# Optimization experiments

Hardware: AMD Instinct MI355X
Metric: run time of the kernel (lower is better)

Reference implementation:

```python
import jax, jax.numpy as jnp
import numpy as np

EPS = 1e-5
MAXN = 1.0 - 1e-5
SEG, T_HORIZONS, MARGIN = 24, 4, 0.1

# --- Poincare ball (c=1) ops ---

def _norm(x):
    return jnp.sqrt(jnp.clip(jnp.sum(x * x, -1, keepdims=True), EPS * EPS, None))

def projx(x):
    n = jnp.sqrt(jnp.clip(jnp.sum(x * x, -1, keepdims=True), EPS * EPS, None))
    return jnp.where(n > MAXN, x * (MAXN / n), x)

def mobius_add(x, y):
    x2 = jnp.sum(x * x, -1, keepdims=True)
    y2 = jnp.sum(y * y, -1, keepdims=True)
    xy = jnp.sum(x * y, -1, keepdims=True)
    num = (1 + 2 * xy + y2) * x + (1 - x2) * y
    den = 1 + 2 * xy + x2 * y2
    return num / jnp.maximum(den, EPS)

def lam(x):
    return 2.0 / jnp.clip(1 - jnp.sum(x * x, -1, keepdims=True), EPS, None)

def expmap(x, v):
    vn = _norm(v)
    return projx(mobius_add(x, jnp.tanh(0.5 * lam(x) * vn) * v / vn))

def logmap(x, y):
    u = mobius_add(-x, y)
    un = _norm(u)
    return (2.0 / lam(x)) * jnp.arctanh(jnp.clip(un, None, MAXN)) * u / un

def expmap0(v):
    vn = _norm(v)
    return projx(jnp.tanh(vn) * v / vn)

def logmap0(x):
    xn = _norm(x)
    return jnp.arctanh(jnp.clip(xn, None, MAXN)) * x / xn

def mob_smul(r, x):
    xn = _norm(x)
    return projx(jnp.tanh(r * jnp.arctanh(jnp.clip(xn, None, MAXN))) * x / xn)

def dist0(x):
    n = jnp.sqrt(jnp.clip(jnp.sum(x * x, -1), EPS * EPS, None))
    return 2.0 * jnp.arctanh(jnp.clip(n, None, MAXN))


def setup_inputs() -> dict:
    key = jax.random.key(0)
    ks = jax.random.split(key, 8)
    B, L, F, D, H = 32, 336, 256, 128, 256
    r = lambda k, s, sc: jax.random.normal(k, s, jnp.float32) * sc
    return {
        "trend": r(ks[0], (B, L, F), 1.0),
        "seasonal_coarse": r(ks[1], (B, L, F), 1.0),
        "seasonal_fine": r(ks[2], (B, L, F), 1.0),
        "residual": r(ks[3], (B, L, F), 1.0),
        "revin_w": jnp.ones((F,), jnp.float32),
        "revin_b": jnp.zeros((F,), jnp.float32),
        "enc_W": r(ks[4], (4, SEG, D), 0.05),
        "enc_b": jnp.zeros((4, D), jnp.float32),
        "vel_W": r(ks[5], (4, D, D), 0.05),
        "vel_b": jnp.zeros((4, D), jnp.float32),
        "steps": jnp.ones((4,), jnp.float32),
        "mobius_w": jnp.full((4,), 0.25, jnp.float32),
        "rec_W1": r(ks[6], (D, H), 0.05),
        "rec_b1": jnp.zeros((H,), jnp.float32),
        "rec_W2": r(ks[7], (H, SEG), 0.05),
        "rec_b2": jnp.zeros((SEG,), jnp.float32),
    }


def reference(trend, seasonal_coarse, seasonal_fine, residual, revin_w, revin_b,
              enc_W, enc_b, vel_W, vel_b, steps, mobius_w,
              rec_W1, rec_b1, rec_W2, rec_b2):
    B, L, F = trend.shape
    N = L // SEG
    # RevIN stats on the combined signal
    x = trend + seasonal_coarse + seasonal_fine + residual
    mean = jnp.mean(x, 1, keepdims=True)                    # [B,1,F]
    std = jnp.sqrt(jnp.var(x, 1, keepdims=True) + 1e-5)

    def collapse(c):
        cn = ((c - 0.25 * mean) / std) * revin_w + 0.25 * revin_b
        return jnp.transpose(cn, (0, 2, 1)).reshape(B * F, N, SEG)

    comps = jnp.stack([collapse(trend), collapse(seasonal_coarse),
                       collapse(seasonal_fine), collapse(residual)])  # [4,BF,N,SEG]

    def branch(xs, We, be, Wv, bv, s):
        z = projx(expmap0(xs @ We + be))                    # [BF,N,D] latents on ball
        v = logmap(z[:, :-1], z[:, 1:])                     # [BF,N-1,D]
        w = 0.9 ** (N - 2 - jnp.arange(N - 1, dtype=xs.dtype))
        w = w / w.sum()
        v_init = jnp.mean(v * w[None, :, None], axis=1)     # weighted then .mean, as in torch
        v0t = projx(expmap0(logmap0(v_init) @ Wv + bv))     # PoincareLinear
        ts = jnp.arange(1, T_HORIZONS + 1, dtype=xs.dtype)
        v_t = jax.nn.sigmoid(s) * ts[None, :, None] * v0t[:, None, :]  # [BF,T,D]
        return expmap(z[:, -1][:, None, :], v_t)            # [BF,T,D]

    z_fut = jax.vmap(branch)(comps, enc_W, enc_b, vel_W, vel_b, steps)  # [4,BF,T,D]

    # Mobius fusion
    w = jax.nn.softmax(mobius_w)
    comb = mob_smul(w[0], z_fut[0])
    for i in range(1, 4):
        comb = mobius_add(comb, mob_smul(w[i], z_fut[i]))
    comb = projx(comb)

    # Reconstruction head: logmap0 -> MLP -> segment values
    h = jax.nn.relu(logmap0(comb) @ rec_W1 + rec_b1)
    seg_out = h @ rec_W2 + rec_b2                           # [BF,T,SEG]
    pred_n = seg_out.reshape(B, F, T_HORIZONS * SEG).transpose(0, 2, 1)  # [B,pred_len,F]
    pred = (pred_n - revin_b) / revin_w * std + mean        # RevIN denorm

    # Hierarchical margin loss on distances from origin
    d = dist0(z_fut)                                        # [4,BF,T]
    hloss = (jnp.mean(jax.nn.relu(d[0] - d[1] + MARGIN)) +
             jnp.mean(jax.nn.relu(d[1] - d[2] + MARGIN)) +
             jnp.mean(jax.nn.relu(d[2] - d[3] + MARGIN)))
    return pred, hloss
```

## Files before the change

### kernel.cpp

```cpp
#include <hip/hip_runtime.h>
#include <math.h>

#define EPSF 1e-5f
#define MAXNF (1.0f - 1e-5f)

constexpr int SEGc = 24;
constexpr int Nn   = 14;
constexpr int NS   = Nn * SEGc;
constexpr int Tt   = 4;
constexpr int Bb   = 32;
constexpr int Ll   = 336;
constexpr int Ff   = 256;
constexpr int Dd   = 128;
constexpr int Hh   = 256;
constexpr int BFc  = Bb * Ff;

constexpr float WNORM = 1.0f / (7.458134171670999f * 13.0f);
constexpr float LN09  = -0.10536051565782628f;

typedef float v2f __attribute__((ext_vector_type(2)));
__device__ __forceinline__ v2f vset(float a, float b){ v2f r; r.x=a; r.y=b; return r; }
__device__ __forceinline__ v2f vsplat(float s){ v2f r; r.x=s; r.y=s; return r; }
__device__ __forceinline__ v2f vfma(v2f a, v2f b, v2f c){
#if __has_builtin(__builtin_elementwise_fma)
    return __builtin_elementwise_fma(a, b, c);
#else
    return vset(fmaf(a.x, b.x, c.x), fmaf(a.y, b.y, c.y));
#endif
}
__device__ __forceinline__ v2f vfmas(float a, v2f b, v2f c){ return vfma(vsplat(a), b, c); }

__device__ __forceinline__ float frcp(float x)  { return __builtin_amdgcn_rcpf(x); }
__device__ __forceinline__ float fsqrtf_(float x){ return __builtin_amdgcn_sqrtf(x); }
__device__ __forceinline__ float ftanh_pos(float x) {
    const float e = __expf(fminf(2.f * x, 30.f));
    return (e - 1.f) * frcp(e + 1.f);
}
__device__ __forceinline__ float fatanh01(float x) {
    return 0.5f * __logf((1.f + x) * frcp(1.f - x));
}

__global__ __launch_bounds__(256, 4) void fused_kernel(
    const float* __restrict__ trend, const float* __restrict__ scoarse,
    const float* __restrict__ sfine, const float* __restrict__ resid,
    const float* __restrict__ revin_w, const float* __restrict__ revin_b,
    const float* __restrict__ enc_W, const float* __restrict__ enc_b,
    const float* __restrict__ vel_W, const float* __restrict__ vel_b,
    const float* __restrict__ steps, const float* __restrict__ mobius_w,
    const float* __restrict__ rec_W1, const float* __restrict__ rec_b1,
    const float* __restrict__ rec_W2, const float* __restrict__ rec_b2,
    float* __restrict__ out, float* __restrict__ hpart)
{
    const int bid   = blockIdx.x;
    const int kpair = ((bid & 7) << 9) | (bid >> 3);
    const int bf0   = kpair << 1;
    const int b     = bf0 >> 8;
    const int f0    = bf0 & 255;
    const int tid   = threadIdx.x;
    const int wid   = tid >> 6;
    const int lane  = tid & 63;
    const int gi    = lane & 15;
    const int pg    = (lane >> 4) & 1;

    __shared__ float lds_big[2 * 4 * Tt * Dd];
    __shared__ float bcu[8 * Dd];
    __shared__ float zfns[2][4][Tt];
    __shared__ float red[16];

#define XS(p, c)     (lds_big + ((p) * 4 + (c)) * NS)
#define ZFL(p, i, t) (lds_big + (((p) * 4 + (i)) * Tt + (t)) * Dd)

    const float* cp = (wid == 0) ? trend : (wid == 1) ? scoarse
                    : (wid == 2) ? sfine : resid;

#pragma unroll 1
    for (int i = lane; i < NS; i += 64) {
        const float2 v = *reinterpret_cast<const float2*>(&cp[(b * Ll + i) * Ff + f0]);
        XS(0, wid)[i] = v.x;
        XS(1, wid)[i] = v.y;
    }
    __syncthreads();

    float s0 = 0.f, q0 = 0.f, s1 = 0.f, q1 = 0.f;
#pragma unroll 1
    for (int l = tid; l < NS; l += 256) {
        const float x0 = XS(0,0)[l] + XS(0,1)[l] + XS(0,2)[l] + XS(0,3)[l];
        const float x1 = XS(1,0)[l] + XS(1,1)[l] + XS(1,2)[l] + XS(1,3)[l];
        s0 += x0; q0 += x0 * x0; s1 += x1; q1 += x1 * x1;
    }
#pragma unroll 1
    for (int off = 1; off < 64; off <<= 1) {
        s0 += __shfl_xor(s0, off, 64); q0 += __shfl_xor(q0, off, 64);
        s1 += __shfl_xor(s1, off, 64); q1 += __shfl_xor(q1, off, 64);
    }
    if (lane == 0) {
        red[wid] = s0; red[4 + wid] = q0; red[8 + wid] = s1; red[12 + wid] = q1;
    }
    __syncthreads();
    s0 = red[0] + red[1] + red[2] + red[3];
    q0 = red[4] + red[5] + red[6] + red[7];
    s1 = red[8] + red[9] + red[10] + red[11];
    q1 = red[12] + red[13] + red[14] + red[15];
    const float mean0 = s0 * (1.f / (float)NS);
    const float stdv0 = fsqrtf_(q0 * (1.f / (float)NS) - mean0 * mean0 + 1e-5f);
    const float mean1 = s1 * (1.f / (float)NS);
    const float stdv1 = fsqrtf_(q1 * (1.f / (float)NS) - mean1 * mean1 + 1e-5f);
    const float rw0v = revin_w[f0],     rb0v = revin_b[f0];
    const float rw1v = revin_w[f0 + 1], rb1v = revin_b[f0 + 1];
    const float aff0 = frcp(stdv0) * rw0v;
    const float kaf0 = 0.25f * (rb0v - mean0 * aff0);
    const float aff1 = frcp(stdv1) * rw1v;
    const float kaf1 = 0.25f * (rb1v - mean1 * aff1);

    const int c = wid;
    const float4* xv40 = reinterpret_cast<const float4*>(XS(0, c));
    const float4* xv41 = reinterpret_cast<const float4*>(XS(1, c));
    const float* Wep = enc_W + c * SEGc * Dd + 2 * lane;
    const float* Wvp = vel_W + c * Dd * Dd + 2 * lane;

    v2f wreg[SEGc];
#pragma unroll
    for (int s = 0; s < SEGc; ++s)
        wreg[s] = *reinterpret_cast<const v2f*>(Wep + s * Dd);
    const v2f bev = *reinterpret_cast<const v2f*>(enc_b + c * Dd + 2 * lane);
    const v2f bvv = *reinterpret_cast<const v2f*>(vel_b + c * Dd + 2 * lane);

    v2f csv = vsplat(0.f);
#pragma unroll
    for (int s = 0; s < SEGc; ++s) csv += wreg[s];
    const v2f kb0v = vfmas(kaf0, csv, bev);
    const v2f kb1v = vfmas(kaf1, csv, bev);

    v2f y0v[Nn], y1v[Nn];
#pragma unroll
    for (int n = 0; n < Nn; ++n) {
        v2f a0 = vsplat(0.f), a1 = vsplat(0.f);
#pragma unroll
        for (int q = 0; q < SEGc / 4; ++q) {
            const float4 xa = xv40[n * (SEGc / 4) + q];
            const float4 xb = xv41[n * (SEGc / 4) + q];
            a0 = vfmas(xa.x, wreg[4*q+0], a0); a1 = vfmas(xb.x, wreg[4*q+0], a1);
            a0 = vfmas(xa.y, wreg[4*q+1], a0); a1 = vfmas(xb.y, wreg[4*q+1], a1);
            a0 = vfmas(xa.z, wreg[4*q+2], a0); a1 = vfmas(xb.z, wreg[4*q+2], a1);
            a0 = vfmas(xa.w, wreg[4*q+3], a0); a1 = vfmas(xb.w, wreg[4*q+3], a1);
        }
        y0v[n] = vfmas(aff0, a0, kb0v);
        y1v[n] = vfmas(aff1, a1, kb1v);
    }

    float qnv[2][Nn], rdv[2][Nn - 1];
#pragma unroll
    for (int n = 0; n < Nn; ++n) {
        qnv[0][n] = fmaf(y0v[n].y, y0v[n].y, y0v[n].x * y0v[n].x);
        qnv[1][n] = fmaf(y1v[n].y, y1v[n].y, y1v[n].x * y1v[n].x);
    }
#pragma unroll
    for (int n = 1; n < Nn; ++n) {
        rdv[0][n - 1] = fmaf(y0v[n-1].y, y0v[n].y, y0v[n-1].x * y0v[n].x);
        rdv[1][n - 1] = fmaf(y1v[n-1].y, y1v[n].y, y1v[n-1].x * y1v[n].x);
    }
#pragma unroll 1
    for (int off = 1; off < 64; off <<= 1) {
#pragma unroll
        for (int n = 0; n < Nn; ++n) {
            qnv[0][n] += __shfl_xor(qnv[0][n], off, 64);
            qnv[1][n] += __shfl_xor(qnv[1][n], off, 64);
        }
#pragma unroll
        for (int j = 0; j < Nn - 1; ++j) {
            rdv[0][j] += __shfl_xor(rdv[0][j], off, 64);
            rdv[1][j] += __shfl_xor(rdv[1][j], off, 64);
        }
    }
    float qsel0 = qnv[0][0], qsel1 = qnv[1][0];
#pragma unroll
    for (int n = 1; n < Nn; ++n) {
        qsel0 = (gi == n) ? qnv[0][n] : qsel0;
        qsel1 = (gi == n) ? qnv[1][n] : qsel1;
    }
    const float qn_own = pg ? qsel1 : qsel0;
    float rsel0 = rdv[0][0], rsel1 = rdv[1][0];
#pragma unroll
    for (int n = 1; n < Nn - 1; ++n) {
        rsel0 = (gi == n) ? rdv[0][n] : rsel0;
        rsel1 = (gi == n) ? rdv[1][n] : rsel1;
    }
    const float rd_own = pg ? rsel1 : rsel0;

    const float vn = fsqrtf_(fmaxf(qn_own, EPSF * EPSF));
    const float th = ftanh_pos(vn);
    float s_own = th * frcp(vn);
    float nrm = th;
    if (nrm > MAXNF) { s_own *= MAXNF * frcp(nrm); nrm = MAXNF; }
    const float zn2_own = nrm * nrm;

    const float s_prev   = __shfl(s_own,   lane - 1, 64);
    const float zn2_prev = __shfl(zn2_own, lane - 1, 64);
    const float rd_prev  = __shfl(rd_own,  lane - 1, 64);

    const float xyv  = -(s_prev * s_own * rd_prev);
    const float x2v  = zn2_prev, yy2 = zn2_own;
    const float c1v  = 1.f + 2.f * xyv + yy2;
    const float c2v  = 1.f - x2v;
    const float rdenv = frcp(fmaxf(1.f + 2.f * xyv + x2v * yy2, EPSF));
    const float un2 = rdenv * rdenv *
        (c1v * c1v * x2v + 2.f * c1v * c2v * xyv + c2v * c2v * yy2);
    const float un  = fsqrtf_(fmaxf(un2, EPSF * EPSF));
    const float lf  = fmaxf(1.f - x2v, EPSF);
    const float gml = lf * fatanh01(fminf(un, MAXNF)) * frcp(un);
    const float wj  = WNORM * __expf(LN09 * (float)(13 - gi));
    const float gw  = wj * gml * rdenv;
    const float g1_own = -gw * c1v * s_prev;
    const float g2_own =  gw * c2v * s_own;

    v2f vi0v = vsplat(0.f), vi1v = vsplat(0.f);
#pragma unroll
    for (int n = 0; n < Nn; ++n) {
        float cf0 = 0.f, cf1 = 0.f;
        if (n >= 1)      { cf0 = __shfl(g2_own, n, 64);       cf1 = __shfl(g2_own, 16 + n, 64); }
        if (n <= Nn - 2) { cf0 += __shfl(g1_own, n + 1, 64);  cf1 += __shfl(g1_own, 17 + n, 64); }
        vi0v = vfmas(cf0, y0v[n], vi0v);
        vi1v = vfmas(cf1, y1v[n], vi1v);
    }
    const float scl0 = __shfl(s_own, 13, 64),  x2l0 = __shfl(zn2_own, 13, 64);
    const float scl1 = __shfl(s_own, 29, 64),  x2l1 = __shfl(zn2_own, 29, 64);
    const v2f z0lv = y0v[Nn-1] * scl0;
    const v2f z1lv = y1v[Nn-1] * scl1;

    float vin20 = fmaf(vi0v.y, vi0v.y, vi0v.x * vi0v.x);
    float vin21 = fmaf(vi1v.y, vi1v.y, vi1v.x * vi1v.x);
#pragma unroll 1
    for (int off = 1; off < 64; off <<= 1) {
        vin20 += __shfl_xor(vin20, off, 64);
        vin21 += __shfl_xor(vin21, off, 64);
    }
    const float vinn0 = fsqrtf_(fmaxf(vin20, EPSF * EPSF));
    const float lgv0  = fatanh01(fminf(vinn0, MAXNF)) * frcp(vinn0);
    const float vinn1 = fsqrtf_(fmaxf(vin21, EPSF * EPSF));
    const float lgv1  = fatanh01(fminf(vinn1, MAXNF)) * frcp(vinn1);
    *reinterpret_cast<v2f*>(&bcu[(0 * 4 + c) * Dd + 2 * lane]) = vi0v * lgv0;
    *reinterpret_cast<v2f*>(&bcu[(4 + c) * Dd + 2 * lane])     = vi1v * lgv1;
    __syncthreads();

    v2f m0v = bvv, m1v = bvv;
    {
        const float4* bc40 = reinterpret_cast<const float4*>(bcu + (0 * 4 + c) * Dd);
        const float4* bc41 = reinterpret_cast<const float4*>(bcu + (4 + c) * Dd);
#pragma unroll 1
        for (int kb = 0; kb < Dd / 8; ++kb) {
            v2f w[8];
#pragma unroll
            for (int r = 0; r < 8; ++r)
                w[r] = *reinterpret_cast<const v2f*>(Wvp + (8 * kb + r) * Dd);
            const float4 ta0 = bc40[2*kb], tb0 = bc40[2*kb+1];
            const float4 ta1 = bc41[2*kb], tb1 = bc41[2*kb+1];
            m0v = vfmas(ta0.x, w[0], m0v); m1v = vfmas(ta1.x, w[0], m1v);
            m0v = vfmas(ta0.y, w[1], m0v); m1v = vfmas(ta1.y, w[1], m1v);
            m0v = vfmas(ta0.z, w[2], m0v); m1v = vfmas(ta1.z, w[2], m1v);
            m0v = vfmas(ta0.w, w[3], m0v); m1v = vfmas(ta1.w, w[3], m1v);
            m0v = vfmas(tb0.x, w[4], m0v); m1v = vfmas(tb1.x, w[4], m1v);
            m0v = vfmas(tb0.y, w[5], m0v); m1v = vfmas(tb1.y, w[5], m1v);
            m0v = vfmas(tb0.z, w[6], m0v); m1v = vfmas(tb1.z, w[6], m1v);
            m0v = vfmas(tb0.w, w[7], m0v); m1v = vfmas(tb1.w, w[7], m1v);
        }
    }
    float mn20 = fmaf(m0v.y, m0v.y, m0v.x * m0v.x);
    float zdm0 = fmaf(z0lv.y, m0v.y, z0lv.x * m0v.x);
    float mn21 = fmaf(m1v.y, m1v.y, m1v.x * m1v.x);
    float zdm1 = fmaf(z1lv.y, m1v.y, z1lv.x * m1v.x);
#pragma unroll 1
    for (int off = 1; off < 64; off <<= 1) {
        mn20 += __shfl_xor(mn20, off, 64); zdm0 += __shfl_xor(zdm0, off, 64);
        mn21 += __shfl_xor(mn21, off, 64); zdm1 += __shfl_xor(zdm1, off, 64);
    }

    const float sig = frcp(1.f + __expf(-steps[c]));
    {
        const float mn2g = pg ? mn21 : mn20;
        const float zdmg = pg ? zdm1 : zdm0;
        const float x2lg = pg ? x2l1 : x2l0;
        const float mng  = fsqrtf_(fmaxf(mn2g, EPSF * EPSF));
        const float thg  = ftanh_pos(mng);
        float sc2g = thg * frcp(mng);
        float v0ng = thg;
        if (v0ng > MAXNF) { sc2g *= MAXNF * frcp(v0ng); v0ng = MAXNF; }
        const float v0n2g  = mn2g * sc2g * sc2g;
        const float zdotvg = sc2g * zdmg;
        const float lamxg  = 2.f * frcp(fmaxf(1.f - x2lg, EPSF));

        const float alpha = sig * (float)(gi + 1);
        const float vtn2  = alpha * alpha * v0n2g;
        const float vtn   = fsqrtf_(fmaxf(vtn2, EPSF * EPSF));
        const float gg    = ftanh_pos(0.5f * lamxg * vtn);
        const float cyc   = gg * alpha * frcp(vtn);
        const float y2    = cyc * cyc * v0n2g;
        const float xy    = cyc * zdotvg;
        const float c1 = 1.f + 2.f * xy + y2;
        const float c2 = 1.f - x2lg;
        const float rden = frcp(fmaxf(1.f + 2.f * xy + x2lg * y2, EPSF));
        float rn2 = rden * rden *
            (c1 * c1 * x2lg + 2.f * c1 * c2 * xy + c2 * c2 * y2);
        float rn = fsqrtf_(fmaxf(rn2, EPSF * EPSF));
        float sclip = 1.f;
        if (rn > MAXNF) { sclip = MAXNF * frcp(rn); rn = MAXNF; }
        const float At_own = c1 * rden * sclip;
        const float Bt_own = c2 * cyc * rden * sclip;
        if (lane < 32 && gi < Tt) zfns[pg][c][gi] = rn;

        const float sc2_0 = __shfl(sc2g, 0, 64), sc2_1 = __shfl(sc2g, 16, 64);
        const v2f v0d0 = m0v * sc2_0;
        const v2f v0d1 = m1v * sc2_1;
#pragma unroll 1
        for (int t = 0; t < Tt; ++t) {
            const float A0 = __shfl(At_own, t, 64),      B0 = __shfl(Bt_own, t, 64);
            const float A1 = __shfl(At_own, 16 + t, 64), B1 = __shfl(Bt_own, 16 + t, 64);
            *reinterpret_cast<v2f*>(ZFL(0, c, t) + 2 * lane) = vfmas(A0, z0lv, v0d0 * B0);
            *reinterpret_cast<v2f*>(ZFL(1, c, t) + 2 * lane) = vfmas(A1, z1lv, v0d1 * B1);
        }
    }
    __syncthreads();

    {
        float mwa = mobius_w[0], mwb = mobius_w[1], mwc = mobius_w[2], mwd = mobius_w[3];
        const float mx = fmaxf(fmaxf(mwa, mwb), fmaxf(mwc, mwd));
        mwa = __expf(mwa - mx); mwb = __expf(mwb - mx);
        mwc = __expf(mwc - mx); mwd = __expf(mwd - mx);
        const float rse = frcp(mwa + mwb + mwc + mwd);
        const float mw[4] = {mwa * rse, mwb * rse, mwc * rse, mwd * rse};

        const int t = wid;
        v2f e0[4], e1[4];
#pragma unroll
        for (int i = 0; i < 4; ++i) {
            e0[i] = *reinterpret_cast<const v2f*>(ZFL(0, i, t) + 2 * lane);
            e1[i] = *reinterpret_cast<const v2f*>(ZFL(1, i, t) + 2 * lane);
        }
        float gp[12];
        gp[0]  = fmaf(e0[0].y, e0[1].y, e0[0].x * e0[1].x);
        gp[1]  = fmaf(e0[0].y, e0[2].y, e0[0].x * e0[2].x);
        gp[2]  = fmaf(e0[0].y, e0[3].y, e0[0].x * e0[3].x);
        gp[3]  = fmaf(e0[1].y, e0[2].y, e0[1].x * e0[2].x);
        gp[4]  = fmaf(e0[1].y, e0[3].y, e0[1].x * e0[3].x);
        gp[5]  = fmaf(e0[2].y, e0[3].y, e0[2].x * e0[3].x);
        gp[6]  = fmaf(e1[0].y, e1[1].y, e1[0].x * e1[1].x);
        gp[7]  = fmaf(e1[0].y, e1[2].y, e1[0].x * e1[2].x);
        gp[8]  = fmaf(e1[0].y, e1[3].y, e1[0].x * e1[3].x);
        gp[9]  = fmaf(e1[1].y, e1[2].y, e1[1].x * e1[2].x);
        gp[10] = fmaf(e1[1].y, e1[3].y, e1[1].x * e1[3].x);
        gp[11] = fmaf(e1[2].y, e1[3].y, e1[2].x * e1[3].x);
#pragma unroll 1
        for (int off = 1; off < 64; off <<= 1) {
#pragma unroll
            for (int k = 0; k < 12; ++k) gp[k] += __shfl_xor(gp[k], off, 64);
        }

        const int il = lane & 3;
        float mwv_own = mw[0];
        mwv_own = (il == 1) ? mw[1] : mwv_own;
        mwv_own = (il == 2) ? mw[2] : mwv_own;
        mwv_own = (il == 3) ? mw[3] : mwv_own;
        const float xn_own = zfns[pg][il][t];
        const float smc = ftanh_pos(mwv_own * fatanh01(xn_own)) * frcp(xn_own);
        float smv[2][4];
#pragma unroll
        for (int i = 0; i < 4; ++i) {
            smv[0][i] = __shfl(smc, i, 64);
            smv[1][i] = __shfl(smc, 16 + i, 64);
        }

#pragma unroll
        for (int p = 0; p < 2; ++p) {
            const float xn0 = zfns[p][0][t], xn1 = zfns[p][1][t];
            const float xn2 = zfns[p][2][t], xn3 = zfns[p][3][t];
            const float Gd[4] = {xn0*xn0, xn1*xn1, xn2*xn2, xn3*xn3};
            const float G[4][4] = {
                {Gd[0], gp[6*p+0], gp[6*p+1], gp[6*p+2]},
                {gp[6*p+0], Gd[1], gp[6*p+3], gp[6*p+4]},
                {gp[6*p+1], gp[6*p+3], Gd[2], gp[6*p+5]},
                {gp[6*p+2], gp[6*p+4], gp[6*p+5], Gd[3]}};
            float a0 = smv[p][0], a1 = 0.f, a2 = 0.f, a3 = 0.f;
            float cn2 = smv[p][0] * smv[p][0] * Gd[0];
#pragma unroll
            for (int i = 1; i < 4; ++i) {
                const float si = smv[p][i];
                const float xy = si * (a0*G[0][i] + a1*G[1][i] + a2*G[2][i] + a3*G[3][i]);
                const float y2 = si * si * Gd[i];
                const float c1 = 1.f + 2.f * xy + y2;
                const float c2 = 1.f - cn2;
                const float rden = frcp(fmaxf(1.f + 2.f * xy + cn2 * y2, EPSF));
                const float f1 = rden * c1, f2 = rden * c2 * si;
                a0 *= f1; a1 *= f1; a2 *= f1; a3 *= f1;
                if (i == 1) a1 += f2; else if (i == 2) a2 += f2; else a3 += f2;
                cn2 = rden * rden * (c1*c1*cn2 + 2.f*c1*c2*xy + c2*c2*y2);
            }
            float cn = fsqrtf_(fmaxf(cn2, EPSF * EPSF));
            float csc = 1.f;
            if (cn > MAXNF) { csc = MAXNF * frcp(cn); cn = MAXNF; }
            const float lg = fatanh01(cn) * frcp(cn) * csc;
            const v2f* ee = p ? e1 : e0;
            v2f uv = ee[0] * a0;
            uv = vfmas(a1, ee[1], uv);
            uv = vfmas(a2, ee[2], uv);
            uv = vfmas(a3, ee[3], uv);
            uv = uv * lg;
            const int ub = (t * Dd + 2 * lane) * 2 + p;
            bcu[ub]     = uv.x;
            bcu[ub + 2] = uv.y;
        }
    }

    if (wid == 0) {
        float ddv = 0.f;
        if (lane < 32)
            ddv = 2.f * fatanh01(zfns[pg][lane & 3][gi >> 2]);
        const float ddn = __shfl(ddv, lane + 1, 64);
        float hv = ((lane < 32) && ((lane & 3) != 3))
                 ? fmaxf(ddv - ddn + 0.1f, 0.f) : 0.f;
#pragma unroll 1
        for (int off = 1; off < 16; off <<= 1) hv += __shfl_xor(hv, off, 64);
        if (lane == 0)  hpart[bf0]     = hv;
        if (lane == 16) hpart[bf0 + 1] = hv;
    }
    __syncthreads();

    {
        const float4* u4 = reinterpret_cast<const float4*>(bcu);
        const float bb = rec_b1[tid];
        v2f accv[4] = {vsplat(bb), vsplat(bb), vsplat(bb), vsplat(bb)};
        const float* w1p = rec_W1 + tid;
#pragma unroll 1
        for (int kb = 0; kb < Dd / 8; ++kb) {
            float wv[8];
#pragma unroll
            for (int r = 0; r < 8; ++r) wv[r] = w1p[(8 * kb + r) * Hh];
#pragma unroll
            for (int rr = 0; rr < 4; ++rr) {
#pragma unroll
                for (int t = 0; t < 4; ++t) {
                    const float4 U = u4[t * (Dd / 2) + 4 * kb + rr];
                    accv[t] = vfmas(wv[2*rr],   vset(U.x, U.y), accv[t]);
                    accv[t] = vfmas(wv[2*rr+1], vset(U.z, U.w), accv[t]);
                }
            }
        }
#pragma unroll
        for (int t = 0; t < 4; ++t) {
            v2f h = vset(fmaxf(accv[t].x, 0.f), fmaxf(accv[t].y, 0.f));
            *reinterpret_cast<v2f*>(lds_big + (t * Hh + tid) * 2) = h;
        }
    }
    __syncthreads();

    if (tid < Tt * SEGc) {
        const int t = tid / SEGc, s = tid - t * SEGc;
        const float4* h4 = reinterpret_cast<const float4*>(lds_big);
        const float* w2p = rec_W2 + s;
        v2f acc2 = vsplat(rec_b2[s]);
#pragma unroll 1
        for (int jb = 0; jb < Hh / 8; ++jb) {
            float wv[8];
#pragma unroll
            for (int r = 0; r < 8; ++r) wv[r] = w2p[(8 * jb + r) * SEGc];
#pragma unroll
            for (int rr = 0; rr < 4; ++rr) {
                const float4 H = h4[t * (Hh / 2) + 4 * jb + rr];
                acc2 = vfmas(wv[2*rr],   vset(H.x, H.y), acc2);
                acc2 = vfmas(wv[2*rr+1], vset(H.z, H.w), acc2);
            }
        }
        const v2f rbv = vset(rb0v, rb1v);
        const v2f rwr = vset(frcp(rw0v), frcp(rw1v));
        const v2f sdv = vset(stdv0, stdv1);
        const v2f mnv = vset(mean0, mean1);
        const v2f res = (acc2 - rbv) * rwr * sdv + mnv;
        *reinterpret_cast<float2*>(&out[(b * (Tt * SEGc) + tid) * Ff + f0]) =
            make_float2(res.x, res.y);
    }
#undef XS
#undef ZFL
}

__global__ __launch_bounds__(256) void hloss_kernel(
    const float* __restrict__ hpart, float* __restrict__ out)
{
    __shared__ float sm[256];
    const int tid = threadIdx.x;
    float s = 0.f;
#pragma unroll 1
    for (int i = tid; i < BFc; i += 256) s += hpart[i];
    sm[tid] = s;
    __syncthreads();
#pragma unroll 1
    for (int off = 128; off > 0; off >>= 1) {
        if (tid < off) sm[tid] += sm[tid + off];
        __syncthreads();
    }
    if (tid == 0) out[Bb * Tt * SEGc * Ff] = sm[0] / (float)(BFc * Tt);
}

extern "C" void kernel_launch(void* const* d_in, const int* in_sizes, int n_in,
                              void* d_out, int out_size, void* d_ws, size_t ws_size,
                              hipStream_t stream) {
    const float* trend   = (const float*)d_in[0];
    const float* scoarse = (const float*)d_in[1];
    const float* sfine   = (const float*)d_in[2];
    const float* resid   = (const float*)d_in[3];
    const float* revin_w = (const float*)d_in[4];
    const float* revin_b = (const float*)d_in[5];
    const float* enc_W   = (const float*)d_in[6];
    const float* enc_b   = (const float*)d_in[7];
    const float* vel_W   = (const float*)d_in[8];
    const float* vel_b   = (const float*)d_in[9];
    const float* steps   = (const float*)d_in[10];
    const float* mobw    = (const float*)d_in[11];
    const float* rec_W1  = (const float*)d_in[12];
    const float* rec_b1  = (const float*)d_in[13];
    const float* rec_W2  = (const float*)d_in[14];
    const float* rec_b2  = (const float*)d_in[15];

    float* out = (float*)d_out;
    float* wsf = (float*)d_ws;

    fused_kernel<<<BFc / 2, 256, 0, stream>>>(
        trend, scoarse, sfine, resid, revin_w, revin_b,
        enc_W, enc_b, vel_W, vel_b, steps, mobw,
        rec_W1, rec_b1, rec_W2, rec_b2,
        out, wsf);
    hloss_kernel<<<1, 256, 0, stream>>>(wsf, out);
}
```

Measured before the change: 221.4 us.

## Have each wave load all four components redundantly to drop block barriers

Every wave now reads all four component inputs for its two features, computes the RevIN sum and sum-of-squares itself with a wave-level reduction, and stores only its own component in a private LDS region. This removes the cross-wave LDS reduction and two __syncthreads, and the LDS layout is changed so that each wave's scratch and z_fut region is separate. In exchange, global load traffic per block is four times higher, though the repeated loads should mostly hit in cache. The barrier before the velocity matvec is also removed, which is safe only because each wave reads only the bcu rows it wrote itself.

```diff
diff --git a/kernel.cpp b/kernel.cpp
--- a/kernel.cpp
+++ b/kernel.cpp
@@ -62,45 +62,42 @@
     const int gi    = lane & 15;
     const int pg    = (lane >> 4) & 1;
 
-    __shared__ float lds_big[2 * 4 * Tt * Dd];
+    __shared__ float lds_big[4 * 1024];
     __shared__ float bcu[8 * Dd];
     __shared__ float zfns[2][4][Tt];
-    __shared__ float red[16];
-
-#define XS(p, c)     (lds_big + ((p) * 4 + (c)) * NS)
-#define ZFL(p, i, t) (lds_big + (((p) * 4 + (i)) * Tt + (t)) * Dd)
-
-    const float* cp = (wid == 0) ? trend : (wid == 1) ? scoarse
-                    : (wid == 2) ? sfine : resid;
-
-#pragma unroll 1
-    for (int i = lane; i < NS; i += 64) {
-        const float2 v = *reinterpret_cast<const float2*>(&cp[(b * Ll + i) * Ff + f0]);
-        XS(0, wid)[i] = v.x;
-        XS(1, wid)[i] = v.y;
-    }
-    __syncthreads();
+
+#define XSW(p)        (lds_big + c * 1024 + (p) * NS)
+#define ZFL2(cc, p, t)(lds_big + (cc) * 1024 + ((p) * 4 + (t)) * Dd)
+
+    const int c = wid;
 
     float s0 = 0.f, q0 = 0.f, s1 = 0.f, q1 = 0.f;
-#pragma unroll 1
-    for (int l = tid; l < NS; l += 256) {
-        const float x0 = XS(0,0)[l] + XS(0,1)[l] + XS(0,2)[l] + XS(0,3)[l];
-        const float x1 = XS(1,0)[l] + XS(1,1)[l] + XS(1,2)[l] + XS(1,3)[l];
-        s0 += x0; q0 += x0 * x0; s1 += x1; q1 += x1 * x1;
+    {
+        float* xs0 = XSW(0);
+        float* xs1 = XSW(1);
+#pragma unroll 1
+        for (int l = lane; l < NS; l += 64) {
+            const int gidx = (b * Ll + l) * Ff + f0;
+            const float2 vt = *reinterpret_cast<const float2*>(&trend[gidx]);
+            const float2 vc = *reinterpret_cast<const float2*>(&scoarse[gidx]);
+            const float2 vf = *reinterpret_cast<const float2*>(&sfine[gidx]);
+            const float2 vr = *reinterpret_cast<const float2*>(&resid[gidx]);
+            const float x0 = vt.x + vc.x + vf.x + vr.x;
+            const float x1 = vt.y + vc.y + vf.y + vr.y;
+            s0 += x0; q0 += x0 * x0; s1 += x1; q1 += x1 * x1;
+            float2 own = vt;
+            own = (c == 1) ? vc : own;
+            own = (c == 2) ? vf : own;
+            own = (c == 3) ? vr : own;
+            xs0[l] = own.x;
+            xs1[l] = own.y;
+        }
     }
 #pragma unroll 1
     for (int off = 1; off < 64; off <<= 1) {
         s0 += __shfl_xor(s0, off, 64); q0 += __shfl_xor(q0, off, 64);
         s1 += __shfl_xor(s1, off, 64); q1 += __shfl_xor(q1, off, 64);
     }
-    if (lane == 0) {
-        red[wid] = s0; red[4 + wid] = q0; red[8 + wid] = s1; red[12 + wid] = q1;
-    }
-    __syncthreads();
-    s0 = red[0] + red[1] + red[2] + red[3];
-    q0 = red[4] + red[5] + red[6] + red[7];
-    s1 = red[8] + red[9] + red[10] + red[11];
-    q1 = red[12] + red[13] + red[14] + red[15];
     const float mean0 = s0 * (1.f / (float)NS);
     const float stdv0 = fsqrtf_(q0 * (1.f / (float)NS) - mean0 * mean0 + 1e-5f);
     const float mean1 = s1 * (1.f / (float)NS);
@@ -112,9 +109,8 @@
     const float aff1 = frcp(stdv1) * rw1v;
     const float kaf1 = 0.25f * (rb1v - mean1 * aff1);
 
-    const int c = wid;
-    const float4* xv40 = reinterpret_cast<const float4*>(XS(0, c));
-    const float4* xv41 = reinterpret_cast<const float4*>(XS(1, c));
+    const float4* xv40 = reinterpret_cast<const float4*>(XSW(0));
+    const float4* xv41 = reinterpret_cast<const float4*>(XSW(1));
     const float* Wep = enc_W + c * SEGc * Dd + 2 * lane;
     const float* Wvp = vel_W + c * Dd * Dd + 2 * lane;
 
@@ -240,7 +236,6 @@
     const float lgv1  = fatanh01(fminf(vinn1, MAXNF)) * frcp(vinn1);
     *reinterpret_cast<v2f*>(&bcu[(0 * 4 + c) * Dd + 2 * lane]) = vi0v * lgv0;
     *reinterpret_cast<v2f*>(&bcu[(4 + c) * Dd + 2 * lane])     = vi1v * lgv1;
-    __syncthreads();
 
     v2f m0v = bvv, m1v = bvv;
     {
@@ -314,8 +309,8 @@
         for (int t = 0; t < Tt; ++t) {
             const float A0 = __shfl(At_own, t, 64),      B0 = __shfl(Bt_own, t, 64);
             const float A1 = __shfl(At_own, 16 + t, 64), B1 = __shfl(Bt_own, 16 + t, 64);
-            *reinterpret_cast<v2f*>(ZFL(0, c, t) + 2 * lane) = vfmas(A0, z0lv, v0d0 * B0);
-            *reinterpret_cast<v2f*>(ZFL(1, c, t) + 2 * lane) = vfmas(A1, z1lv, v0d1 * B1);
+            *reinterpret_cast<v2f*>(ZFL2(c, 0, t) + 2 * lane) = vfmas(A0, z0lv, v0d0 * B0);
+            *reinterpret_cast<v2f*>(ZFL2(c, 1, t) + 2 * lane) = vfmas(A1, z1lv, v0d1 * B1);
         }
     }
     __syncthreads();
@@ -332,8 +327,8 @@
         v2f e0[4], e1[4];
 #pragma unroll
         for (int i = 0; i < 4; ++i) {
-            e0[i] = *reinterpret_cast<const v2f*>(ZFL(0, i, t) + 2 * lane);
-            e1[i] = *reinterpret_cast<const v2f*>(ZFL(1, i, t) + 2 * lane);
+            e0[i] = *reinterpret_cast<const v2f*>(ZFL2(i, 0, t) + 2 * lane);
+            e1[i] = *reinterpret_cast<const v2f*>(ZFL2(i, 1, t) + 2 * lane);
         }
         float gp[12];
         gp[0]  = fmaf(e0[0].y, e0[1].y, e0[0].x * e0[1].x);
@@ -476,8 +471,8 @@
         *reinterpret_cast<float2*>(&out[(b * (Tt * SEGc) + tid) * Ff + f0]) =
             make_float2(res.x, res.y);
     }
-#undef XS
-#undef ZFL
+#undef XSW
+#undef ZFL2
 }
 
 __global__ __launch_bounds__(256) void hloss_kernel(
```

Result: slower. 238.1 us (+7.5%).
